# Kernel optimization log

Measured on AMD Instinct MI355X. Metric: run time of the kernel, lower is better.

## Reference

```python
import jax, jax.numpy as jnp
import numpy as np

N_HEAD = 16
LORA_SCALE = 1.0 / 4.0  # alpha=1, r=4
LN_EPS = 1e-5


def _ln(x, g, b):
    # LayerNorm subclass casts to float32 then back to input dtype
    xf = x.astype(jnp.float32)
    m = xf.mean(-1, keepdims=True)
    v = xf.var(-1, keepdims=True)
    y = (xf - m) / jnp.sqrt(v + LN_EPS) * g + b
    return y.astype(x.dtype)


def _lora(h, a, b):
    # x @ a.T @ b.T * scaling ; a:[r,d], b:[d,r]
    return (h @ a.T) @ b.T * LORA_SCALE


def _attn(h, Wq, bq, Wk, Wv, bv, Wo, bo, la_k, lb_k, la_v, lb_v, la_o, lb_o):
    B, S, D = h.shape
    hd = D // N_HEAD
    scale = hd ** (-0.25)
    q = h @ Wq.T + bq
    k = h @ Wk.T + _lora(h, la_k, lb_k)          # key Linear has no bias
    v = h @ Wv.T + bv + _lora(h, la_v, lb_v)
    qh = q.reshape(B, S, N_HEAD, hd).transpose(0, 2, 1, 3) * scale  # [B,H,S,hd]
    kh = k.reshape(B, S, N_HEAD, hd).transpose(0, 2, 1, 3) * scale
    vh = v.reshape(B, S, N_HEAD, hd).transpose(0, 2, 1, 3)
    qk = jnp.einsum('bhqd,bhkd->bhqk', qh, kh).astype(jnp.float32)
    w = jax.nn.softmax(qk, axis=-1).astype(q.dtype)
    wv = jnp.einsum('bhqk,bhkd->bhqd', w, vh)
    wv = wv.transpose(0, 2, 1, 3).reshape(B, S, D)
    return wv @ Wo.T + bo + _lora(wv, la_o, lb_o)


def setup_inputs() -> dict:
    key = jax.random.key(0)
    D, R = 1024, 4
    B, S = 8, 1024
    ks = jax.random.split(key, 20)
    sd = 0.02
    inp = {
        'x': jax.random.normal(ks[0], (B, S, D), jnp.float32),
        'Wq': jax.random.normal(ks[1], (D, D), jnp.float32) * sd,
        'bq': jnp.zeros((D,), jnp.float32),
        'Wk': jax.random.normal(ks[2], (D, D), jnp.float32) * sd,
        'Wv': jax.random.normal(ks[3], (D, D), jnp.float32) * sd,
        'bv': jnp.zeros((D,), jnp.float32),
        'Wo': jax.random.normal(ks[4], (D, D), jnp.float32) * sd,
        'bo': jnp.zeros((D,), jnp.float32),
        'la_k': jax.random.normal(ks[5], (R, D), jnp.float32) * sd,
        'lb_k': jax.random.normal(ks[6], (D, R), jnp.float32) * sd,
        'la_v': jax.random.normal(ks[7], (R, D), jnp.float32) * sd,
        'lb_v': jax.random.normal(ks[8], (D, R), jnp.float32) * sd,
        'la_o': jax.random.normal(ks[9], (R, D), jnp.float32) * sd,
        'lb_o': jax.random.normal(ks[10], (D, R), jnp.float32) * sd,
        'g_attn': jnp.ones((D,), jnp.float32),
        'b_attn': jnp.zeros((D,), jnp.float32),
        'W1': jax.random.normal(ks[11], (4 * D, D), jnp.float32) * sd,
        'b1': jnp.zeros((4 * D,), jnp.float32),
        'W2': jax.random.normal(ks[12], (D, 4 * D), jnp.float32) * sd,
        'b2': jnp.zeros((D,), jnp.float32),
        'g_mlp': jnp.ones((D,), jnp.float32),
        'b_mlp': jnp.zeros((D,), jnp.float32),
    }
    return inp


def reference(x, Wq, bq, Wk, Wv, bv, Wo, bo, la_k, lb_k, la_v, lb_v, la_o, lb_o,
              g_attn, b_attn, W1, b1, W2, b2, g_mlp, b_mlp):
    # self-attention + residual (LoRA on key/value/out)
    x = x + _attn(_ln(x, g_attn, b_attn), Wq, bq, Wk, Wv, bv, Wo, bo,
                  la_k, lb_k, la_v, lb_v, la_o, lb_o)
    # MLP + residual (exact GELU, matching nn.GELU default)
    h = _ln(x, g_mlp, b_mlp)
    h = jax.nn.gelu(h @ W1.T + b1, approximate=False)
    x = x + h @ W2.T + b2
    return x
```

## Files before the change

kernel.cpp:

```cpp
#include <hip/hip_runtime.h>
#include <math.h>

typedef _Float16 f16_t;
typedef f16_t f16x8 __attribute__((ext_vector_type(8)));
typedef f16_t f16x4 __attribute__((ext_vector_type(4)));
typedef float f32x4 __attribute__((ext_vector_type(4)));
typedef float fv4 __attribute__((ext_vector_type(4)));

#define MFMA16(a, b, c) __builtin_amdgcn_mfma_f32_16x16x32_f16(a, b, c, 0, 0, 0)

__device__ __forceinline__ void gload16(const void* g, void* l) {
  __builtin_amdgcn_global_load_lds((const __attribute__((address_space(1))) void*)g,
                                   (__attribute__((address_space(3))) void*)l, 16, 0, 0);
}

__global__ __launch_bounds__(256) void ln_f32(const float* __restrict__ x,
                                              const float* __restrict__ g,
                                              const float* __restrict__ b,
                                              f16_t* __restrict__ y) {
  const int D = 1024;
  int row = blockIdx.x;
  int t = threadIdx.x;
  const float* xr = x + (size_t)row * D + t * 4;
  float x0 = xr[0], x1 = xr[1], x2 = xr[2], x3 = xr[3];
  float sum = x0 + x1 + x2 + x3;
  float sq = x0 * x0 + x1 * x1 + x2 * x2 + x3 * x3;
  for (int d = 32; d; d >>= 1) {
    sum += __shfl_down(sum, d);
    sq += __shfl_down(sq, d);
  }
  __shared__ float ssum[4], ssq[4];
  int w = t >> 6, lane = t & 63;
  if (lane == 0) { ssum[w] = sum; ssq[w] = sq; }
  __syncthreads();
  float ts = ssum[0] + ssum[1] + ssum[2] + ssum[3];
  float tq = ssq[0] + ssq[1] + ssq[2] + ssq[3];
  float mean = ts * (1.0f / 1024.0f);
  float var = tq * (1.0f / 1024.0f) - mean * mean;
  float rstd = rsqrtf(var + 1e-5f);
  f16_t* yr = y + (size_t)row * D + t * 4;
  const float* gr = g + t * 4;
  const float* br = b + t * 4;
  yr[0] = (f16_t)((x0 - mean) * rstd * gr[0] + br[0]);
  yr[1] = (f16_t)((x1 - mean) * rstd * gr[1] + br[1]);
  yr[2] = (f16_t)((x2 - mean) * rstd * gr[2] + br[2]);
  yr[3] = (f16_t)((x3 - mean) * rstd * gr[3] + br[3]);
}

__global__ __launch_bounds__(256) void ln_f16(const f16_t* __restrict__ x,
                                              const float* __restrict__ g,
                                              const float* __restrict__ b,
                                              f16_t* __restrict__ y) {
  const int D = 1024;
  int row = blockIdx.x;
  int t = threadIdx.x;
  const f16_t* xr = x + (size_t)row * D + t * 4;
  float x0 = (float)xr[0], x1 = (float)xr[1], x2 = (float)xr[2], x3 = (float)xr[3];
  float sum = x0 + x1 + x2 + x3;
  float sq = x0 * x0 + x1 * x1 + x2 * x2 + x3 * x3;
  for (int d = 32; d; d >>= 1) {
    sum += __shfl_down(sum, d);
    sq += __shfl_down(sq, d);
  }
  __shared__ float ssum[4], ssq[4];
  int w = t >> 6, lane = t & 63;
  if (lane == 0) { ssum[w] = sum; ssq[w] = sq; }
  __syncthreads();
  float ts = ssum[0] + ssum[1] + ssum[2] + ssum[3];
  float tq = ssq[0] + ssq[1] + ssq[2] + ssq[3];
  float mean = ts * (1.0f / 1024.0f);
  float var = tq * (1.0f / 1024.0f) - mean * mean;
  float rstd = rsqrtf(var + 1e-5f);
  f16_t* yr = y + (size_t)row * D + t * 4;
  const float* gr = g + t * 4;
  const float* br = b + t * 4;
  yr[0] = (f16_t)((x0 - mean) * rstd * gr[0] + br[0]);
  yr[1] = (f16_t)((x1 - mean) * rstd * gr[1] + br[1]);
  yr[2] = (f16_t)((x2 - mean) * rstd * gr[2] + br[2]);
  yr[3] = (f16_t)((x3 - mean) * rstd * gr[3] + br[3]);
}

__global__ __launch_bounds__(256) void lora_t_kernel(const f16_t* __restrict__ h,
                                                     const float* __restrict__ la,
                                                     float* __restrict__ t, int K) {
  int lane = threadIdx.x & 63;
  int w = threadIdx.x >> 6;
  int row = blockIdx.x * 4 + w;
  const f16_t* hrow = h + (size_t)row * K;
  float acc[4] = {0.f, 0.f, 0.f, 0.f};
  for (int it = 0; it < K / 512; ++it) {
    int base = it * 512 + lane * 8;
    f16x8 hx = *(const f16x8*)(hrow + base);
#pragma unroll
    for (int r = 0; r < 4; ++r) {
      const float* ar = la + (size_t)r * K + base;
#pragma unroll
      for (int j = 0; j < 8; ++j) acc[r] += (float)hx[j] * ar[j];
    }
  }
#pragma unroll
  for (int r = 0; r < 4; ++r) {
    for (int d = 32; d; d >>= 1) acc[r] += __shfl_down(acc[r], d);
  }
  if (lane == 0) {
#pragma unroll
    for (int r = 0; r < 4; ++r) t[(size_t)row * 4 + r] = acc[r];
  }
}

__global__ __launch_bounds__(256, 2) void gemm_mfma(
    const f16_t* __restrict__ A, const float* __restrict__ B,
    const float* __restrict__ bias, const float* __restrict__ loraT,
    const float* __restrict__ loraB, const float* residf,
    const f16_t* __restrict__ residb, f16_t* Cb, float* Cf, f16_t* Cvt,
    int M, int N, int K, int ldb, int dogelu) {
  __shared__ __align__(16) f16_t smem[2][16384];
  const int tid = threadIdx.x;
  const int lane = tid & 63, wid = tid >> 6;
  const int wm = wid >> 1, wn = wid & 1;
  const int l15 = lane & 15, lhi = lane >> 4;
  const int m0 = blockIdx.y * 128, n0 = blockIdx.x * 128;
  const int arow = tid >> 3;
  const int aslot = tid & 7;

  f32x4 acc[4][4];
#pragma unroll
  for (int i = 0; i < 4; ++i)
#pragma unroll
    for (int j = 0; j < 4; ++j) acc[i][j] = (f32x4){0.f, 0.f, 0.f, 0.f};

  fv4 breg[4][2];

  auto stageA = [&](int step, int buf) {
#pragma unroll
    for (int c = 0; c < 4; ++c) {
      int r = c * 32 + arow;
      int cm = aslot ^ (r & 7);
      gload16(A + (size_t)(m0 + r) * K + (size_t)step * 64 + cm * 8,
              (char*)&smem[buf][0] + c * 4096 + wid * 1024);
    }
  };
  auto loadB = [&](int step) {
#pragma unroll
    for (int c = 0; c < 4; ++c) {
      int r = c * 32 + arow;
      const float* gp = B + (size_t)(n0 + r) * ldb + (size_t)step * 64 + aslot * 8;
      breg[c][0] = *(const fv4*)gp;
      breg[c][1] = *(const fv4*)(gp + 4);
    }
  };
  auto writeB = [&](int buf) {
#pragma unroll
    for (int c = 0; c < 4; ++c) {
      int r = c * 32 + arow;
      f16x8 hh;
#pragma unroll
      for (int j = 0; j < 4; ++j) hh[j] = (f16_t)breg[c][0][j];
#pragma unroll
      for (int j = 0; j < 4; ++j) hh[4 + j] = (f16_t)breg[c][1][j];
      int boff = r * 128 + ((aslot * 16) ^ ((r & 7) << 4));
      *(f16x8*)((char*)&smem[buf][8192] + boff) = hh;
    }
  };

  const int nsteps = K >> 6;
  stageA(0, 0);
  loadB(0);
  writeB(0);
  __syncthreads();
  for (int t = 0; t < nsteps; ++t) {
    int cur = t & 1, nxt = cur ^ 1;
    if (t + 1 < nsteps) { stageA(t + 1, nxt); loadB(t + 1); }
    const char* As = (const char*)&smem[cur][0];
    const char* Bs = (const char*)&smem[cur][8192];
#pragma unroll
    for (int kk = 0; kk < 2; ++kk) {
      f16x8 af[4], bf[4];
#pragma unroll
      for (int i = 0; i < 4; ++i) {
        int row = wm * 64 + i * 16 + l15;
        af[i] = *(const f16x8*)(As + row * 128 + ((kk * 64 + lhi * 16) ^ ((row & 7) << 4)));
      }
#pragma unroll
      for (int j = 0; j < 4; ++j) {
        int row = wn * 64 + j * 16 + l15;
        bf[j] = *(const f16x8*)(Bs + row * 128 + ((kk * 64 + lhi * 16) ^ ((row & 7) << 4)));
      }
#pragma unroll
      for (int i = 0; i < 4; ++i)
#pragma unroll
        for (int j = 0; j < 4; ++j) acc[i][j] = MFMA16(af[i], bf[j], acc[i][j]);
    }
    if (t + 1 < nsteps) writeB(nxt);
    __syncthreads();
  }

  const int gm = m0 + wm * 64, gn = n0 + wn * 64;
#pragma unroll
  for (int j = 0; j < 4; ++j) {
    int gcol = gn + j * 16 + l15;
    float bj = bias ? bias[gcol] : 0.f;
    float lb0 = 0.f, lb1 = 0.f, lb2 = 0.f, lb3 = 0.f;
    if (loraB) {
      const float* p = loraB + (size_t)gcol * 4;
      lb0 = p[0]; lb1 = p[1]; lb2 = p[2]; lb3 = p[3];
    }
#pragma unroll
    for (int i = 0; i < 4; ++i) {
      float v4[4];
#pragma unroll
      for (int r = 0; r < 4; ++r) {
        int grow = gm + i * 16 + lhi * 4 + r;
        float val = acc[i][j][r] + bj;
        if (loraT) {
          const float* tp = loraT + (size_t)grow * 4;
          val += 0.25f * (tp[0] * lb0 + tp[1] * lb1 + tp[2] * lb2 + tp[3] * lb3);
        }
        if (dogelu) val = 0.5f * val * (1.0f + erff(val * 0.70710678118654752f));
        if (residf) val += residf[(size_t)grow * N + gcol];
        if (residb) val += (float)residb[(size_t)grow * N + gcol];
        v4[r] = val;
      }
      if (Cf) {
#pragma unroll
        for (int r = 0; r < 4; ++r)
          Cf[(size_t)(gm + i * 16 + lhi * 4 + r) * N + gcol] = v4[r];
      } else if (Cvt) {
        int grow0 = gm + i * 16 + lhi * 4;
        int bb = grow0 >> 10, ss = grow0 & 1023;
        int hh = gcol >> 6, dd = gcol & 63;
        f16x4 pk;
#pragma unroll
        for (int r = 0; r < 4; ++r) pk[r] = (f16_t)v4[r];
        *(f16x4*)(Cvt + (((size_t)bb * 16 + hh) * 64 + dd) * 1024 + ss) = pk;
      } else {
#pragma unroll
        for (int r = 0; r < 4; ++r)
          Cb[(size_t)(gm + i * 16 + lhi * 4 + r) * N + gcol] = (f16_t)v4[r];
      }
    }
  }
}

__global__ __launch_bounds__(256, 2) void attn_mfma(const f16_t* __restrict__ q,
                                                    const f16_t* __restrict__ k,
                                                    const f16_t* __restrict__ vt,
                                                    f16_t* __restrict__ wv) {
  const int S = 1024, D = 1024;
  __shared__ __align__(16) f16_t Qs[128 * 64];
  __shared__ __align__(16) f16_t SP[128 * 64];
  __shared__ __align__(16) f16_t Ks[64 * 64];
  __shared__ __align__(16) f16_t Vts[64 * 64];
  __shared__ float rsb[128];
  __shared__ float lib[128];
  const int tid = threadIdx.x, lane = tid & 63, w = tid >> 6;
  const int l15 = lane & 15, lhi = lane >> 4;
  const int q0 = blockIdx.x * 128;
  const int h = blockIdx.y, b = blockIdx.z;
  const f16_t* qg = q + ((size_t)b * S + q0) * D + h * 64;
  const f16_t* kg = k + (size_t)b * S * D + h * 64;
  const f16_t* vg = vt + ((size_t)b * 16 + h) * 64 * (size_t)S;

#pragma unroll
  for (int c = 0; c < 4; ++c) {
    int r = c * 32 + (tid >> 3), kc = tid & 7;
    f16x8 xx = *(const f16x8*)(qg + (size_t)r * D + kc * 8);
    *(f16x8*)((char*)Qs + r * 128 + ((kc * 16) ^ ((r & 7) << 4))) = xx;
  }
  __syncthreads();
  f16x8 qf[2][2];
#pragma unroll
  for (int i = 0; i < 2; ++i) {
    int row = w * 32 + i * 16 + l15;
#pragma unroll
    for (int kk = 0; kk < 2; ++kk)
      qf[i][kk] = *(const f16x8*)((char*)Qs + row * 128 +
                                  ((kk * 64 + lhi * 16) ^ ((row & 7) << 4)));
  }

  f32x4 oacc[2][4];
#pragma unroll
  for (int i = 0; i < 2; ++i)
#pragma unroll
    for (int j = 0; j < 4; ++j) oacc[i][j] = (f32x4){0.f, 0.f, 0.f, 0.f};
  float m_run = -1e30f, l_run = 0.f;
  const int myrow = w * 32 + (lane >> 1);
  const int half = lane & 1;

  for (int kv = 0; kv < 16; ++kv) {
    __syncthreads();
#pragma unroll
    for (int c = 0; c < 2; ++c) {
      int r = c * 32 + (tid >> 3), kc = tid & 7;
      f16x8 xk = *(const f16x8*)(kg + (size_t)(kv * 64 + r) * D + kc * 8);
      *(f16x8*)((char*)Ks + r * 128 + ((kc * 16) ^ ((r & 7) << 4))) = xk;
      f16x8 xv = *(const f16x8*)(vg + (size_t)r * S + kv * 64 + kc * 8);
      *(f16x8*)((char*)Vts + r * 128 + ((kc * 16) ^ ((r & 7) << 4))) = xv;
    }
    __syncthreads();
    f32x4 sacc[2][4];
#pragma unroll
    for (int i = 0; i < 2; ++i)
#pragma unroll
      for (int j = 0; j < 4; ++j) sacc[i][j] = (f32x4){0.f, 0.f, 0.f, 0.f};
#pragma unroll
    for (int kk = 0; kk < 2; ++kk) {
      f16x8 kf[4];
#pragma unroll
      for (int j = 0; j < 4; ++j) {
        int row = j * 16 + l15;
        kf[j] = *(const f16x8*)((char*)Ks + row * 128 +
                                ((kk * 64 + lhi * 16) ^ ((row & 7) << 4)));
      }
#pragma unroll
      for (int i = 0; i < 2; ++i)
#pragma unroll
        for (int j = 0; j < 4; ++j) sacc[i][j] = MFMA16(qf[i][kk], kf[j], sacc[i][j]);
    }
#pragma unroll
    for (int i = 0; i < 2; ++i)
#pragma unroll
      for (int j = 0; j < 4; ++j)
#pragma unroll
        for (int r = 0; r < 4; ++r) {
          int srow = w * 32 + i * 16 + lhi * 4 + r;
          int scol = j * 16 + l15;
          *(f16_t*)((char*)SP + srow * 128 + ((scol * 2) ^ ((srow & 7) << 4))) =
              (f16_t)(sacc[i][j][r] * 0.125f);
        }
    __syncthreads();
    f16x8 ch[4];
#pragma unroll
    for (int c = 0; c < 4; ++c)
      ch[c] = *(const f16x8*)((char*)SP + myrow * 128 +
                              ((half * 64 + c * 16) ^ ((myrow & 7) << 4)));
    float mt = -1e30f;
#pragma unroll
    for (int c = 0; c < 4; ++c)
#pragma unroll
      for (int e = 0; e < 8; ++e) mt = fmaxf(mt, (float)ch[c][e]);
    mt = fmaxf(mt, __shfl_xor(mt, 1));
    float mnew = fmaxf(m_run, mt);
    float resc = __expf(m_run - mnew);
    float lsum = 0.f;
#pragma unroll
    for (int c = 0; c < 4; ++c) {
      f16x8 p8;
#pragma unroll
      for (int e = 0; e < 8; ++e) {
        float p = __expf((float)ch[c][e] - mnew);
        lsum += p;
        p8[e] = (f16_t)p;
      }
      *(f16x8*)((char*)SP + myrow * 128 + ((half * 64 + c * 16) ^ ((myrow & 7) << 4))) = p8;
    }
    lsum += __shfl_xor(lsum, 1);
    l_run = l_run * resc + lsum;
    m_run = mnew;
    if (half == 0) rsb[myrow] = resc;
    __syncthreads();
#pragma unroll
    for (int i = 0; i < 2; ++i) {
      float f0 = rsb[w * 32 + i * 16 + lhi * 4 + 0];
      float f1 = rsb[w * 32 + i * 16 + lhi * 4 + 1];
      float f2 = rsb[w * 32 + i * 16 + lhi * 4 + 2];
      float f3 = rsb[w * 32 + i * 16 + lhi * 4 + 3];
#pragma unroll
      for (int j = 0; j < 4; ++j) {
        oacc[i][j][0] *= f0;
        oacc[i][j][1] *= f1;
        oacc[i][j][2] *= f2;
        oacc[i][j][3] *= f3;
      }
    }
#pragma unroll
    for (int kk = 0; kk < 2; ++kk) {
      f16x8 pa[2], vb[4];
#pragma unroll
      for (int i = 0; i < 2; ++i) {
        int row = w * 32 + i * 16 + l15;
        pa[i] = *(const f16x8*)((char*)SP + row * 128 +
                                ((kk * 64 + lhi * 16) ^ ((row & 7) << 4)));
      }
#pragma unroll
      for (int j = 0; j < 4; ++j) {
        int row = j * 16 + l15;
        vb[j] = *(const f16x8*)((char*)Vts + row * 128 +
                                ((kk * 64 + lhi * 16) ^ ((row & 7) << 4)));
      }
#pragma unroll
      for (int i = 0; i < 2; ++i)
#pragma unroll
        for (int j = 0; j < 4; ++j) oacc[i][j] = MFMA16(pa[i], vb[j], oacc[i][j]);
    }
  }
  if (half == 0) lib[myrow] = 1.f / l_run;
  __syncthreads();
#pragma unroll
  for (int i = 0; i < 2; ++i)
#pragma unroll
    for (int r = 0; r < 4; ++r) {
      int row = w * 32 + i * 16 + lhi * 4 + r;
      float li = lib[row];
      size_t base = ((size_t)b * S + q0 + row) * D + h * 64;
#pragma unroll
      for (int j = 0; j < 4; ++j)
        wv[base + j * 16 + l15] = (f16_t)(oacc[i][j][r] * li);
    }
}

extern "C" void kernel_launch(void* const* d_in, const int* in_sizes, int n_in,
                              void* d_out, int out_size, void* d_ws, size_t ws_size,
                              hipStream_t stream) {
  const int B = 8, S = 1024, D = 1024, F = 4096;
  const int M = B * S;

  const float* x = (const float*)d_in[0];
  const float* Wq = (const float*)d_in[1];
  const float* bq = (const float*)d_in[2];
  const float* Wk = (const float*)d_in[3];
  const float* Wv = (const float*)d_in[4];
  const float* bv = (const float*)d_in[5];
  const float* Wo = (const float*)d_in[6];
  const float* bo = (const float*)d_in[7];
  const float* la_k = (const float*)d_in[8];
  const float* lb_k = (const float*)d_in[9];
  const float* la_v = (const float*)d_in[10];
  const float* lb_v = (const float*)d_in[11];
  const float* la_o = (const float*)d_in[12];
  const float* lb_o = (const float*)d_in[13];
  const float* g_attn = (const float*)d_in[14];
  const float* b_attn = (const float*)d_in[15];
  const float* W1 = (const float*)d_in[16];
  const float* b1 = (const float*)d_in[17];
  const float* W2 = (const float*)d_in[18];
  const float* b2 = (const float*)d_in[19];
  const float* g_mlp = (const float*)d_in[20];
  const float* b_mlp = (const float*)d_in[21];

  float* t_k = (float*)((char*)d_ws + 16);
  float* t_v = t_k + (size_t)M * 4;
  float* t_o = t_v + (size_t)M * 4;
  const size_t MD = (size_t)M * D;
  f16_t* P0 = (f16_t*)((char*)d_ws + 409600);
  f16_t* P1 = P0 + MD;
  f16_t* P2 = P0 + 2 * MD;
  f16_t* P3 = P0 + 3 * MD;
  float* outf = (float*)d_out;

  ln_f32<<<M, 256, 0, stream>>>(x, g_attn, b_attn, P0);
  lora_t_kernel<<<M / 4, 256, 0, stream>>>(P0, la_k, t_k, D);
  lora_t_kernel<<<M / 4, 256, 0, stream>>>(P0, la_v, t_v, D);
  gemm_mfma<<<dim3(8, 64), 256, 0, stream>>>(
      P0, Wq, bq, nullptr, nullptr, nullptr, nullptr, P1, nullptr, nullptr,
      M, D, D, D, 0);
  gemm_mfma<<<dim3(8, 64), 256, 0, stream>>>(
      P0, Wk, nullptr, t_k, lb_k, nullptr, nullptr, P2, nullptr, nullptr,
      M, D, D, D, 0);
  gemm_mfma<<<dim3(8, 64), 256, 0, stream>>>(
      P0, Wv, bv, t_v, lb_v, nullptr, nullptr, nullptr, nullptr, P3,
      M, D, D, D, 0);
  attn_mfma<<<dim3(8, 16, 8), 256, 0, stream>>>(P1, P2, P3, P0);
  lora_t_kernel<<<M / 4, 256, 0, stream>>>(P0, la_o, t_o, D);
  gemm_mfma<<<dim3(8, 64), 256, 0, stream>>>(
      P0, Wo, bo, t_o, lb_o, x, nullptr, P3, nullptr, nullptr, M, D, D, D, 0);
  ln_f16<<<M, 256, 0, stream>>>(P3, g_mlp, b_mlp, P0);
  gemm_mfma<<<dim3(16, 64), 256, 0, stream>>>(
      P0, W1, b1, nullptr, nullptr, nullptr, nullptr, P1, nullptr, nullptr,
      M, 2048, D, D, 1);
  gemm_mfma<<<dim3(8, 64), 256, 0, stream>>>(
      P1, W2, b2, nullptr, nullptr, nullptr, P3, nullptr, outf, nullptr,
      M, D, 2048, F, 0);
  gemm_mfma<<<dim3(16, 64), 256, 0, stream>>>(
      P0, W1 + (size_t)2048 * D, b1 + 2048, nullptr, nullptr, nullptr, nullptr,
      P1, nullptr, nullptr, M, 2048, D, D, 1);
  gemm_mfma<<<dim3(8, 64), 256, 0, stream>>>(
      P1, W2 + 2048, nullptr, nullptr, nullptr, outf, nullptr, nullptr, outf,
      nullptr, M, D, 2048, F, 0);
}
```

Before: 734.2 us.

## Pre-convert weights to fp16 and use async LDS-loading GEMM with block swizzle

Adds a kernel that converts all fp32 weight matrices to fp16 in workspace each call. A new GEMM then loads both A and B tiles directly into LDS with global_load_lds, using an XOR swizzle and a grouped block-index remap for L2 locality, instead of converting fp32 B tiles inside the GEMM. Attention occupancy is also raised to 3 blocks per SM. The trade is an extra conversion pass over about 24MB of weights, and a fallback to the old path when the workspace is too small.

```diff
diff --git a/kernel.cpp b/kernel.cpp
--- a/kernel.cpp
+++ b/kernel.cpp
@@ -80,6 +80,35 @@
   yr[3] = (f16_t)((x3 - mean) * rstd * gr[3] + br[3]);
 }
 
+__global__ __launch_bounds__(256) void convert_w(
+    const float* __restrict__ wq, const float* __restrict__ wk,
+    const float* __restrict__ wv, const float* __restrict__ wo,
+    const float* __restrict__ w1, const float* __restrict__ w2,
+    f16_t* __restrict__ oq, f16_t* __restrict__ ok, f16_t* __restrict__ ov,
+    f16_t* __restrict__ oo, f16_t* __restrict__ o1, f16_t* __restrict__ o2) {
+  int bid = blockIdx.x;
+  const float* src;
+  f16_t* dst;
+  int bi;
+  if (bid < 2048) {
+    int seg = bid >> 9;
+    bi = bid & 511;
+    src = seg == 0 ? wq : seg == 1 ? wk : seg == 2 ? wv : wo;
+    dst = seg == 0 ? oq : seg == 1 ? ok : seg == 2 ? ov : oo;
+  } else if (bid < 4096) {
+    bi = bid - 2048; src = w1; dst = o1;
+  } else {
+    bi = bid - 4096; src = w2; dst = o2;
+  }
+  size_t idx = (size_t)bi * 2048 + (size_t)threadIdx.x * 8;
+  fv4 a = *(const fv4*)(src + idx);
+  fv4 b = *(const fv4*)(src + idx + 4);
+  f16x8 h;
+#pragma unroll
+  for (int j = 0; j < 4; ++j) { h[j] = (f16_t)a[j]; h[4 + j] = (f16_t)b[j]; }
+  *(f16x8*)(dst + idx) = h;
+}
+
 __global__ __launch_bounds__(256) void lora_t_kernel(const f16_t* __restrict__ h,
                                                      const float* __restrict__ la,
                                                      float* __restrict__ t, int K) {
@@ -105,6 +134,120 @@
   if (lane == 0) {
 #pragma unroll
     for (int r = 0; r < 4; ++r) t[(size_t)row * 4 + r] = acc[r];
+  }
+}
+
+__global__ __launch_bounds__(256, 2) void gemm_f16(
+    const f16_t* __restrict__ A, const f16_t* __restrict__ B,
+    const float* __restrict__ bias, const float* __restrict__ loraT,
+    const float* __restrict__ loraB, const float* residf,
+    const f16_t* __restrict__ residb, f16_t* Cb, float* Cf, f16_t* Cvt,
+    int M, int N, int K, int ldb, int dogelu) {
+  __shared__ __align__(16) f16_t smem[2][16384];
+  const int tid = threadIdx.x;
+  const int lane = tid & 63, wid = tid >> 6;
+  const int wm = wid >> 1, wn = wid & 1;
+  const int l15 = lane & 15, lhi = lane >> 4;
+  int nwg = gridDim.x * gridDim.y;
+  int bid = blockIdx.y * gridDim.x + blockIdx.x;
+  int swz = (bid & 7) * (nwg >> 3) + (bid >> 3);
+  const int m0 = (swz / gridDim.x) * 128, n0 = (swz % gridDim.x) * 128;
+  const int arow = tid >> 3;
+  const int aslot = tid & 7;
+
+  f32x4 acc[4][4];
+#pragma unroll
+  for (int i = 0; i < 4; ++i)
+#pragma unroll
+    for (int j = 0; j < 4; ++j) acc[i][j] = (f32x4){0.f, 0.f, 0.f, 0.f};
+
+  auto stage = [&](const f16_t* G, int r0, int ldg, int step, char* lds) {
+#pragma unroll
+    for (int c = 0; c < 4; ++c) {
+      int r = c * 32 + arow;
+      int cm = aslot ^ (r & 7);
+      gload16(G + (size_t)(r0 + r) * ldg + (size_t)step * 64 + cm * 8,
+              lds + c * 4096 + wid * 1024);
+    }
+  };
+
+  const int nsteps = K >> 6;
+  stage(A, m0, K, 0, (char*)&smem[0][0]);
+  stage(B, n0, ldb, 0, (char*)&smem[0][8192]);
+  __syncthreads();
+  for (int t = 0; t < nsteps; ++t) {
+    int cur = t & 1, nxt = cur ^ 1;
+    if (t + 1 < nsteps) {
+      stage(A, m0, K, t + 1, (char*)&smem[nxt][0]);
+      stage(B, n0, ldb, t + 1, (char*)&smem[nxt][8192]);
+    }
+    const char* As = (const char*)&smem[cur][0];
+    const char* Bs = (const char*)&smem[cur][8192];
+#pragma unroll
+    for (int kk = 0; kk < 2; ++kk) {
+      f16x8 af[4], bf[4];
+#pragma unroll
+      for (int i = 0; i < 4; ++i) {
+        int row = wm * 64 + i * 16 + l15;
+        af[i] = *(const f16x8*)(As + row * 128 + ((kk * 64 + lhi * 16) ^ ((row & 7) << 4)));
+      }
+#pragma unroll
+      for (int j = 0; j < 4; ++j) {
+        int row = wn * 64 + j * 16 + l15;
+        bf[j] = *(const f16x8*)(Bs + row * 128 + ((kk * 64 + lhi * 16) ^ ((row & 7) << 4)));
+      }
+#pragma unroll
+      for (int i = 0; i < 4; ++i)
+#pragma unroll
+        for (int j = 0; j < 4; ++j) acc[i][j] = MFMA16(af[i], bf[j], acc[i][j]);
+    }
+    __syncthreads();
+  }
+
+  const int gm = m0 + wm * 64, gn = n0 + wn * 64;
+#pragma unroll
+  for (int j = 0; j < 4; ++j) {
+    int gcol = gn + j * 16 + l15;
+    float bj = bias ? bias[gcol] : 0.f;
+    float lb0 = 0.f, lb1 = 0.f, lb2 = 0.f, lb3 = 0.f;
+    if (loraB) {
+      const float* p = loraB + (size_t)gcol * 4;
+      lb0 = p[0]; lb1 = p[1]; lb2 = p[2]; lb3 = p[3];
+    }
+#pragma unroll
+    for (int i = 0; i < 4; ++i) {
+      float v4[4];
+#pragma unroll
+      for (int r = 0; r < 4; ++r) {
+        int grow = gm + i * 16 + lhi * 4 + r;
+        float val = acc[i][j][r] + bj;
+        if (loraT) {
+          const float* tp = loraT + (size_t)grow * 4;
+          val += 0.25f * (tp[0] * lb0 + tp[1] * lb1 + tp[2] * lb2 + tp[3] * lb3);
+        }
+        if (dogelu) val = 0.5f * val * (1.0f + erff(val * 0.70710678118654752f));
+        if (residf) val += residf[(size_t)grow * N + gcol];
+        if (residb) val += (float)residb[(size_t)grow * N + gcol];
+        v4[r] = val;
+      }
+      if (Cf) {
+#pragma unroll
+        for (int r = 0; r < 4; ++r)
+          Cf[(size_t)(gm + i * 16 + lhi * 4 + r) * N + gcol] = v4[r];
+      } else if (Cvt) {
+        int grow0 = gm + i * 16 + lhi * 4;
+        int bb = grow0 >> 10, ss = grow0 & 1023;
+        int hh = gcol >> 6, dd = gcol & 63;
+        f16x4 pk;
+#pragma unroll
+        for (int r = 0; r < 4; ++r) pk[r] = (f16_t)v4[r];
+        *(f16x4*)(Cvt + (((size_t)bb * 16 + hh) * 64 + dd) * 1024 + ss) = pk;
+      } else {
+#pragma unroll
+        for (int r = 0; r < 4; ++r)
+          Cb[(size_t)(gm + i * 16 + lhi * 4 + r) * N + gcol] = (f16_t)v4[r];
+      }
+    }
   }
 }
 
@@ -242,7 +385,7 @@
   }
 }
 
-__global__ __launch_bounds__(256, 2) void attn_mfma(const f16_t* __restrict__ q,
+__global__ __launch_bounds__(256, 3) void attn_mfma(const f16_t* __restrict__ q,
                                                     const f16_t* __restrict__ k,
                                                     const f16_t* __restrict__ vt,
                                                     f16_t* __restrict__ wv) {
@@ -446,35 +589,79 @@
   f16_t* P1 = P0 + MD;
   f16_t* P2 = P0 + 2 * MD;
   f16_t* P3 = P0 + 3 * MD;
+  f16_t* Wqf = P0 + 4 * MD;
+  f16_t* Wkf = Wqf + (size_t)D * D;
+  f16_t* Wvf = Wkf + (size_t)D * D;
+  f16_t* Wof = Wvf + (size_t)D * D;
+  f16_t* W1f = Wof + (size_t)D * D;
+  f16_t* W2f = W1f + (size_t)F * D;
   float* outf = (float*)d_out;
+  const size_t need = 409600 + 4 * MD * sizeof(f16_t) +
+                      (4 * (size_t)D * D + 2 * (size_t)F * D) * sizeof(f16_t);
+  const bool f16w = ws_size >= need;
+
+  if (f16w)
+    convert_w<<<6144, 256, 0, stream>>>(Wq, Wk, Wv, Wo, W1, W2,
+                                        Wqf, Wkf, Wvf, Wof, W1f, W2f);
 
   ln_f32<<<M, 256, 0, stream>>>(x, g_attn, b_attn, P0);
   lora_t_kernel<<<M / 4, 256, 0, stream>>>(P0, la_k, t_k, D);
   lora_t_kernel<<<M / 4, 256, 0, stream>>>(P0, la_v, t_v, D);
-  gemm_mfma<<<dim3(8, 64), 256, 0, stream>>>(
-      P0, Wq, bq, nullptr, nullptr, nullptr, nullptr, P1, nullptr, nullptr,
-      M, D, D, D, 0);
-  gemm_mfma<<<dim3(8, 64), 256, 0, stream>>>(
-      P0, Wk, nullptr, t_k, lb_k, nullptr, nullptr, P2, nullptr, nullptr,
-      M, D, D, D, 0);
-  gemm_mfma<<<dim3(8, 64), 256, 0, stream>>>(
-      P0, Wv, bv, t_v, lb_v, nullptr, nullptr, nullptr, nullptr, P3,
-      M, D, D, D, 0);
+  if (f16w) {
+    gemm_f16<<<dim3(8, 64), 256, 0, stream>>>(
+        P0, Wqf, bq, nullptr, nullptr, nullptr, nullptr, P1, nullptr, nullptr,
+        M, D, D, D, 0);
+    gemm_f16<<<dim3(8, 64), 256, 0, stream>>>(
+        P0, Wkf, nullptr, t_k, lb_k, nullptr, nullptr, P2, nullptr, nullptr,
+        M, D, D, D, 0);
+    gemm_f16<<<dim3(8, 64), 256, 0, stream>>>(
+        P0, Wvf, bv, t_v, lb_v, nullptr, nullptr, nullptr, nullptr, P3,
+        M, D, D, D, 0);
+  } else {
+    gemm_mfma<<<dim3(8, 64), 256, 0, stream>>>(
+        P0, Wq, bq, nullptr, nullptr, nullptr, nullptr, P1, nullptr, nullptr,
+        M, D, D, D, 0);
+    gemm_mfma<<<dim3(8, 64), 256, 0, stream>>>(
+        P0, Wk, nullptr, t_k, lb_k, nullptr, nullptr, P2, nullptr, nullptr,
+        M, D, D, D, 0);
+    gemm_mfma<<<dim3(8, 64), 256, 0, stream>>>(
+        P0, Wv, bv, t_v, lb_v, nullptr, nullptr, nullptr, nullptr, P3,
+        M, D, D, D, 0);
+  }
   attn_mfma<<<dim3(8, 16, 8), 256, 0, stream>>>(P1, P2, P3, P0);
   lora_t_kernel<<<M / 4, 256, 0, stream>>>(P0, la_o, t_o, D);
-  gemm_mfma<<<dim3(8, 64), 256, 0, stream>>>(
-      P0, Wo, bo, t_o, lb_o, x, nullptr, P3, nullptr, nullptr, M, D, D, D, 0);
+  if (f16w)
+    gemm_f16<<<dim3(8, 64), 256, 0, stream>>>(
+        P0, Wof, bo, t_o, lb_o, x, nullptr, P3, nullptr, nullptr, M, D, D, D, 0);
+  else
+    gemm_mfma<<<dim3(8, 64), 256, 0, stream>>>(
+        P0, Wo, bo, t_o, lb_o, x, nullptr, P3, nullptr, nullptr, M, D, D, D, 0);
   ln_f16<<<M, 256, 0, stream>>>(P3, g_mlp, b_mlp, P0);
-  gemm_mfma<<<dim3(16, 64), 256, 0, stream>>>(
-      P0, W1, b1, nullptr, nullptr, nullptr, nullptr, P1, nullptr, nullptr,
-      M, 2048, D, D, 1);
-  gemm_mfma<<<dim3(8, 64), 256, 0, stream>>>(
-      P1, W2, b2, nullptr, nullptr, nullptr, P3, nullptr, outf, nullptr,
-      M, D, 2048, F, 0);
-  gemm_mfma<<<dim3(16, 64), 256, 0, stream>>>(
-      P0, W1 + (size_t)2048 * D, b1 + 2048, nullptr, nullptr, nullptr, nullptr,
-      P1, nullptr, nullptr, M, 2048, D, D, 1);
-  gemm_mfma<<<dim3(8, 64), 256, 0, stream>>>(
-      P1, W2 + 2048, nullptr, nullptr, nullptr, outf, nullptr, nullptr, outf,
-      nullptr, M, D, 2048, F, 0);
-}
+  if (f16w) {
+    gemm_f16<<<dim3(16, 64), 256, 0, stream>>>(
+        P0, W1f, b1, nullptr, nullptr, nullptr, nullptr, P1, nullptr, nullptr,
+        M, 2048, D, D, 1);
+    gemm_f16<<<dim3(8, 64), 256, 0, stream>>>(
+        P1, W2f, b2, nullptr, nullptr, nullptr, P3, nullptr, outf, nullptr,
+        M, D, 2048, F, 0);
+    gemm_f16<<<dim3(16, 64), 256, 0, stream>>>(
+        P0, W1f + (size_t)2048 * D, b1 + 2048, nullptr, nullptr, nullptr, nullptr,
+        P1, nullptr, nullptr, M, 2048, D, D, 1);
+    gemm_f16<<<dim3(8, 64), 256, 0, stream>>>(
+        P1, W2f + 2048, nullptr, nullptr, nullptr, outf, nullptr, nullptr, outf,
+        nullptr, M, D, 2048, F, 0);
+  } else {
+    gemm_mfma<<<dim3(16, 64), 256, 0, stream>>>(
+        P0, W1, b1, nullptr, nullptr, nullptr, nullptr, P1, nullptr, nullptr,
+        M, 2048, D, D, 1);
+    gemm_mfma<<<dim3(8, 64), 256, 0, stream>>>(
+        P1, W2, b2, nullptr, nullptr, nullptr, P3, nullptr, outf, nullptr,
+        M, D, 2048, F, 0);
+    gemm_mfma<<<dim3(16, 64), 256, 0, stream>>>(
+        P0, W1 + (size_t)2048 * D, b1 + 2048, nullptr, nullptr, nullptr, nullptr,
+        P1, nullptr, nullptr, M, 2048, D, D, 1);
+    gemm_mfma<<<dim3(8, 64), 256, 0, stream>>>(
+        P1, W2 + 2048, nullptr, nullptr, nullptr, outf, nullptr, nullptr, outf,
+        nullptr, M, D, 2048, F, 0);
+  }
+}
```

Measured after the change: 662.5 us. 1.11x faster.
